# Kernel tuning notes

Measured on AMD Instinct MI355X. Metric: run time of the kernel, lower is better.

## Reference

```python
import jax, jax.numpy as jnp
import numpy as np

E = 800_000    # num elements
N = 400_000    # num nodes
NEN = 3        # nodes per element (linear triangle)
NQP = 1        # quadrature points per element
NST = 1        # state variables per quad point
DT = 0.0
MATS = ((1.0, 0.5), (2.0, 1.0))  # (lam, mu) for block0, block1


def _element_energy(elDisp, elCoords, elState, elShapes, elShapeGrads, elVols, lam, mu):
    # FunctionSpace.integrate_element_from_local_field with a Neo-Hookean
    # Lagrangian L(U, gradU, Q, X, dt) = W(gradU, Q); modify_element_gradient = identity.
    def qp(shape, grad, vol, Q):
        gradU = jnp.einsum('nc,nd->cd', elDisp, grad)            # [2,2] displacement gradient
        F = jnp.eye(2, dtype=elDisp.dtype) + gradU
        J = F[0, 0] * F[1, 1] - F[0, 1] * F[1, 0]
        logJ = jnp.log(J)
        I1 = jnp.sum(F * F)
        mu_eff = mu * (1.0 + 0.01 * Q[0])                        # internal variable modulates stiffness
        W = 0.5 * mu_eff * (I1 - 2.0 - 2.0 * logJ) + 0.5 * lam * logJ * logJ
        return W * vol
    return jnp.sum(jax.vmap(qp)(elShapes, elShapeGrads, elVols, elState))


def _block_hessians(U, coords, state, conns, shapes, shapeGrads, vols, elemIds, lam, mu):
    # gather per-block element fields, hessian-of-energy per element, vmapped
    def elem(elConn, elState, elShapes, elShapeGrads, elVols):
        elCoords = coords[elConn]                                # [NEN,2]
        f = lambda d: _element_energy(d, elCoords, elState, elShapes, elShapeGrads, elVols, lam, mu)
        return jax.hessian(f)(U[elConn])                         # [NEN,2,NEN,2]
    return jax.vmap(elem)(conns[elemIds], state[elemIds], shapes[elemIds],
                          shapeGrads[elemIds], vols[elemIds])


def setup_inputs() -> dict:
    key = jax.random.key(0)
    ks = jax.random.split(key, 8)
    U = 0.01 * jax.random.normal(ks[0], (N, 2), jnp.float32)     # small disp -> det(F) > 0
    coords = jax.random.uniform(ks[1], (N, 2), dtype=jnp.float32)
    state = jax.random.uniform(ks[2], (E, NQP, NST), dtype=jnp.float32)
    conns = jax.random.randint(ks[3], (E, NEN), 0, N, dtype=jnp.int32)
    shapes = jax.random.uniform(ks[4], (E, NQP, NEN), dtype=jnp.float32)
    shapeGrads = jax.random.normal(ks[5], (E, NQP, NEN, 2), jnp.float32)
    vols = jax.random.uniform(ks[6], (E, NQP), dtype=jnp.float32)
    perm = jax.random.permutation(ks[7], E)                      # disjoint material blocks
    blocks0 = perm[: E // 2].astype(jnp.int32)
    blocks1 = perm[E // 2:].astype(jnp.int32)
    return dict(U=U, coords=coords, state=state, conns=conns, shapes=shapes,
                shapeGrads=shapeGrads, vols=vols, blocks0=blocks0, blocks1=blocks1)


def reference(U, coords, state, conns, shapes, shapeGrads, vols, blocks0, blocks1):
    # compute_element_stiffnesses: gather -> per-element hessian -> scatter per block
    hess = jnp.zeros((E, NEN, 2, NEN, 2), dtype=U.dtype)
    for blk, (lam, mu) in zip((blocks0, blocks1), MATS):
        bh = _block_hessians(U, coords, state, conns, shapes, shapeGrads, vols, blk, lam, mu)
        hess = hess.at[blk].set(bh)
    return hess
```

## Files before the change

kernel.cpp:

```cpp
#include <hip/hip_runtime.h>


constexpr int E_CNT  = 800000;
constexpr int HALF_E = 400000;

__global__ __launch_bounds__(256) void zero_flags_kernel(uint4* __restrict__ flag4) {
  int i = blockIdx.x * blockDim.x + threadIdx.x;
  if (i < E_CNT / 16) flag4[i] = make_uint4(0, 0, 0, 0);
}

__global__ __launch_bounds__(256) void mark_b1_kernel(
    const int* __restrict__ b1, unsigned char* __restrict__ flag) {
  int i = blockIdx.x * blockDim.x + threadIdx.x;
  if (i < HALF_E) flag[b1[i]] = 1;
}

__global__ __launch_bounds__(256) void hess_kernel(
    const float* __restrict__ U, const float* __restrict__ state,
    const int* __restrict__ conns, const float* __restrict__ grads,
    const float* __restrict__ vols, const unsigned char* __restrict__ flag,
    float* __restrict__ out) {
  __shared__ float lds[256 * 37];
  const int tid = threadIdx.x;
  const int e = blockIdx.x * 256 + tid;

  const bool b  = flag[e] != 0;
  const float lam = b ? 2.0f : 1.0f;
  const float mu  = b ? 1.0f : 0.5f;

  const int n0 = conns[3 * e + 0];
  const int n1 = conns[3 * e + 1];
  const int n2 = conns[3 * e + 2];
  const float2 d0 = *(const float2*)(U + 2 * n0);
  const float2 d1 = *(const float2*)(U + 2 * n1);
  const float2 d2 = *(const float2*)(U + 2 * n2);
  const float2* gp = (const float2*)(grads + 6 * e);
  const float2 g0 = gp[0], g1 = gp[1], g2 = gp[2];

  const float gu00 = d0.x * g0.x + d1.x * g1.x + d2.x * g2.x;
  const float gu01 = d0.x * g0.y + d1.x * g1.y + d2.x * g2.y;
  const float gu10 = d0.y * g0.x + d1.y * g1.x + d2.y * g2.x;
  const float gu11 = d0.y * g0.y + d1.y * g1.y + d2.y * g2.y;

  const float F00 = 1.0f + gu00, F01 = gu01, F10 = gu10, F11 = 1.0f + gu11;
  const float J    = F00 * F11 - F01 * F10;
  const float logJ = logf(J);
  const float rJ   = 1.0f / J;
  const float Fi00 =  F11 * rJ, Fi01 = -F01 * rJ;
  const float Fi10 = -F10 * rJ, Fi11 =  F00 * rJ;

  float P[3][2];
  P[0][0] = g0.x * Fi00 + g0.y * Fi10;  P[0][1] = g0.x * Fi01 + g0.y * Fi11;
  P[1][0] = g1.x * Fi00 + g1.y * Fi10;  P[1][1] = g1.x * Fi01 + g1.y * Fi11;
  P[2][0] = g2.x * Fi00 + g2.y * Fi10;  P[2][1] = g2.x * Fi01 + g2.y * Fi11;

  const float gx[3] = {g0.x, g1.x, g2.x};
  const float gy[3] = {g0.y, g1.y, g2.y};

  const float mu_eff = mu * (1.0f + 0.01f * state[e]);
  const float c2     = mu_eff - lam * logJ;
  const float vol    = vols[e];

  float* hl = lds + tid * 37;
#pragma unroll
  for (int n = 0; n < 3; ++n) {
#pragma unroll
    for (int m = 0; m < 3; ++m) {
      const float dg = gx[n] * gx[m] + gy[n] * gy[m];
#pragma unroll
      for (int c = 0; c < 2; ++c) {
#pragma unroll
        for (int d = 0; d < 2; ++d) {
          float v = c2 * P[n][d] * P[m][c] + lam * P[n][c] * P[m][d];
          if (c == d) v += mu_eff * dg;
          hl[n * 12 + c * 6 + m * 2 + d] = vol * v;
        }
      }
    }
  }

  __syncthreads();

  float4* ob = (float4*)(out + 36 * (size_t)(blockIdx.x * 256));
#pragma unroll
  for (int i = 0; i < 9; ++i) {
    const int f = 4 * (tid + i * 256);
    float4 v;
    v.x = lds[(f + 0) + (f + 0) / 36];
    v.y = lds[(f + 1) + (f + 1) / 36];
    v.z = lds[(f + 2) + (f + 2) / 36];
    v.w = lds[(f + 3) + (f + 3) / 36];
    ob[tid + i * 256] = v;
  }
}

extern "C" void kernel_launch(void* const* d_in, const int* in_sizes, int n_in,
                              void* d_out, int out_size, void* d_ws, size_t ws_size,
                              hipStream_t stream) {
  const float* U     = (const float*)d_in[0];
  const float* state = (const float*)d_in[2];
  const int*   conns = (const int*)d_in[3];
  const float* grads = (const float*)d_in[5];
  const float* vols  = (const float*)d_in[6];
  const int*   b1    = (const int*)d_in[8];
  float* out = (float*)d_out;
  unsigned char* flag = (unsigned char*)d_ws;

  zero_flags_kernel<<<(E_CNT / 16 + 255) / 256, 256, 0, stream>>>((uint4*)flag);
  mark_b1_kernel<<<(HALF_E + 255) / 256, 256, 0, stream>>>(b1, flag);
  hess_kernel<<<E_CNT / 256, 256, 0, stream>>>(U, state, conns, grads,
                                               vols, flag, out);
}
```

Measured before the change: 190.5 us.

## Halve LDS staging buffer with two-pass transpose and nontemporal float2 stores

Each thread now keeps its 36-entry Hessian in registers, and the block writes it out in two passes through a 128-element LDS buffer instead of one 256-element buffer. This halves shared memory per block, allowing more resident blocks per CU. Output stores become float2 nontemporal writes so the large streaming output does not pollute cache. The cost is an extra barrier, more register pressure from holding 36 values, and narrower stores than the previous float4.

```diff
diff --git a/kernel.cpp b/kernel.cpp
--- a/kernel.cpp
+++ b/kernel.cpp
@@ -3,6 +3,8 @@
 
 constexpr int E_CNT  = 800000;
 constexpr int HALF_E = 400000;
+
+typedef float v2f __attribute__((ext_vector_type(2)));
 
 __global__ __launch_bounds__(256) void zero_flags_kernel(uint4* __restrict__ flag4) {
   int i = blockIdx.x * blockDim.x + threadIdx.x;
@@ -20,7 +22,7 @@
     const int* __restrict__ conns, const float* __restrict__ grads,
     const float* __restrict__ vols, const unsigned char* __restrict__ flag,
     float* __restrict__ out) {
-  __shared__ float lds[256 * 37];
+  __shared__ float lds[128 * 37];
   const int tid = threadIdx.x;
   const int e = blockIdx.x * 256 + tid;
 
@@ -61,7 +63,7 @@
   const float c2     = mu_eff - lam * logJ;
   const float vol    = vols[e];
 
-  float* hl = lds + tid * 37;
+  float h[36];
 #pragma unroll
   for (int n = 0; n < 3; ++n) {
 #pragma unroll
@@ -73,24 +75,34 @@
         for (int d = 0; d < 2; ++d) {
           float v = c2 * P[n][d] * P[m][c] + lam * P[n][c] * P[m][d];
           if (c == d) v += mu_eff * dg;
-          hl[n * 12 + c * 6 + m * 2 + d] = vol * v;
+          h[n * 12 + c * 6 + m * 2 + d] = vol * v;
         }
       }
     }
   }
 
-  __syncthreads();
-
-  float4* ob = (float4*)(out + 36 * (size_t)(blockIdx.x * 256));
+  const size_t blk_base = 36 * (size_t)(blockIdx.x * 256);
 #pragma unroll
-  for (int i = 0; i < 9; ++i) {
-    const int f = 4 * (tid + i * 256);
-    float4 v;
-    v.x = lds[(f + 0) + (f + 0) / 36];
-    v.y = lds[(f + 1) + (f + 1) / 36];
-    v.z = lds[(f + 2) + (f + 2) / 36];
-    v.w = lds[(f + 3) + (f + 3) / 36];
-    ob[tid + i * 256] = v;
+  for (int p = 0; p < 2; ++p) {
+    if (p) __syncthreads();
+    if ((tid >> 7) == p) {
+      float* hl = lds + (tid & 127) * 37;
+#pragma unroll
+      for (int q = 0; q < 36; ++q) hl[q] = h[q];
+    }
+    __syncthreads();
+    float* ob = out + blk_base + p * 4608;
+#pragma unroll
+    for (int i = 0; i < 9; ++i) {
+      const int g = tid + i * 256;
+      const int f = 2 * g;
+      const int el = f / 36;
+      const int j  = f - 36 * el;
+      v2f v;
+      v.x = lds[el * 37 + j];
+      v.y = lds[el * 37 + j + 1];
+      __builtin_nontemporal_store(v, (v2f*)(ob + f));
+    }
   }
 }
 
```

Result: slower. 194.5 us (+2.1%).
